# Optimization experiments

Measured on AMD Instinct MI355X. Metric: run time of the kernel, lower is better.

Reference implementation:

```python
import jax, jax.numpy as jnp
import numpy as np

SEG_LENS = (2048, 4096, 8192)
DIL_RATES = (1, 2, 4)
NUM_HEADS = 12
HEAD_DIM = 64
LN_EPS = 1e-5


def _dilated_attention(q, k, v):
    # q,k,v: [b, n, h, d]; heads partitioned across (segment, dilation) groups
    b, n, h, d = q.shape
    G = len(SEG_LENS)
    hg = h // G
    scale = d ** -0.5
    out = jnp.zeros_like(q)
    for i, (s, r) in enumerate(zip(SEG_LENS, DIL_RATES)):
        hmin = i * hg
        m = n // s                      # number of segments
        idx = jnp.arange(i % r, s, r)   # dilated positions within a segment, len = s // r
        def seg(t):
            # [b, n, hg, d] -> [b, m, s//r, hg, d]
            return t[:, :, hmin:hmin + hg, :].reshape(b, m, s, hg, d)[:, :, idx]
        qs, ks, vs = seg(q), seg(k), seg(v)
        scores = jnp.einsum('bmshd,bmthd->bmhst', qs, ks) * scale  # [b,m,hg,s/r,s/r]
        attn = jax.nn.softmax(scores, axis=-1)
        o = jnp.einsum('bmhst,bmthd->bmshd', attn, vs)              # [b,m,s/r,hg,d]
        pos = (jnp.arange(m)[:, None] * s + idx[None, :]).reshape(-1)
        out = out.at[:, pos, hmin:hmin + hg, :].set(o.reshape(b, -1, hg, d))
    return out


def setup_inputs() -> dict:
    key = jax.random.key(0)
    ks = jax.random.split(key, 4)
    E = NUM_HEADS * HEAD_DIM
    b, n = 1, 8192
    x = jax.random.normal(ks[0], (b, n, E), dtype=jnp.float32)
    w_qkv = jax.random.normal(ks[1], (3 * E, E), dtype=jnp.float32) * (E ** -0.5)
    b_qkv = jnp.zeros((3 * E,), dtype=jnp.float32)
    w_out = jax.random.normal(ks[2], (E, E), dtype=jnp.float32) * (E ** -0.5)
    b_out = jnp.zeros((E,), dtype=jnp.float32)
    ln_gamma = jnp.ones((E,), dtype=jnp.float32)
    ln_beta = jnp.zeros((E,), dtype=jnp.float32)
    return {'x': x, 'w_qkv': w_qkv, 'b_qkv': b_qkv, 'w_out': w_out,
            'b_out': b_out, 'ln_gamma': ln_gamma, 'ln_beta': ln_beta}


def reference(x, w_qkv, b_qkv, w_out, b_out, ln_gamma, ln_beta):
    b, n, E = x.shape
    qkv = x @ w_qkv.T + b_qkv
    q, k, v = jnp.split(qkv, 3, axis=-1)
    shp = (b, n, NUM_HEADS, HEAD_DIM)
    o = _dilated_attention(q.reshape(shp), k.reshape(shp), v.reshape(shp)).reshape(b, n, E)
    # MAGNETO: LayerNorm on attention output before out projection
    mu = jnp.mean(o, axis=-1, keepdims=True)
    var = jnp.mean(jnp.square(o - mu), axis=-1, keepdims=True)
    on = (o - mu) / jnp.sqrt(var + LN_EPS) * ln_gamma + ln_beta
    return on @ w_out.T + b_out
```

## Files before the change

kernel.cpp:

```cpp
#include <hip/hip_runtime.h>
#include <hip/hip_bf16.h>
#include <cstdint>
#include <cstddef>


typedef __attribute__((ext_vector_type(8))) short short8;
typedef __attribute__((ext_vector_type(4))) short short4_;
typedef __attribute__((ext_vector_type(4))) float float4_;

#if __has_builtin(__builtin_amdgcn_exp2f)
#define EXP2(x) __builtin_amdgcn_exp2f(x)
#else
#define EXP2(x) exp2f(x)
#endif

__device__ __forceinline__ float bf2f(short s) {
    unsigned int u = ((unsigned int)(unsigned short)s) << 16;
    float f;
    __builtin_memcpy(&f, &u, 4);
    return f;
}
__device__ __forceinline__ short f2bf(float f) {
    unsigned int u;
    __builtin_memcpy(&u, &f, 4);
    u += 0x7fffu + ((u >> 16) & 1u);
    return (short)(u >> 16);
}
__device__ __forceinline__ short f2bf_trunc(float f) {
    unsigned int u;
    __builtin_memcpy(&u, &f, 4);
    return (short)(u >> 16);
}
__device__ __forceinline__ short8 f8_to_bf8(const float* __restrict__ p) {
    float4_ a = *(const float4_*)(p);
    float4_ b = *(const float4_*)(p + 4);
    short8 r;
    r[0] = f2bf(a[0]); r[1] = f2bf(a[1]); r[2] = f2bf(a[2]); r[3] = f2bf(a[3]);
    r[4] = f2bf(b[0]); r[5] = f2bf(b[1]); r[6] = f2bf(b[2]); r[7] = f2bf(b[3]);
    return r;
}
__device__ __forceinline__ void gll16(const short* g, short* l) {
    __builtin_amdgcn_global_load_lds(
        (const __attribute__((address_space(1))) unsigned int*)g,
        (__attribute__((address_space(3))) unsigned int*)l, 16, 0, 0);
}

#define LDT 72

__global__ __launch_bounds__(256) void cvt3(
    const float* __restrict__ a, int na, const float* __restrict__ b, int nb,
    const float* __restrict__ c, int nc,
    short* __restrict__ oa, short* __restrict__ ob, short* __restrict__ oc)
{
    int i = (blockIdx.x * 256 + threadIdx.x) * 8;
    if (i < na) {
        *(short8*)&oa[i] = f8_to_bf8(a + i);
    } else if (i < na + nb) {
        int j = i - na;
        *(short8*)&ob[j] = f8_to_bf8(b + j);
    } else {
        int j = i - na - nb;
        if (j < nc) *(short8*)&oc[j] = f8_to_bf8(c + j);
    }
}

template<int EPI>
__global__ __launch_bounds__(256) void gemm128(
    const short* __restrict__ A, int lda,
    const short* __restrict__ B,
    const float* __restrict__ bias,
    void* __restrict__ Cv,
    int N, int K)
{
    __shared__ short As[128 * 64];
    __shared__ short Bs[128 * 64];
    const int tid  = threadIdx.x;
    const int wave = tid >> 6, lane = tid & 63;
    const int quad = lane >> 4, l16 = lane & 15;
    const int wr = wave >> 1, wc = wave & 1;
    const int m0 = blockIdx.y * 128, n0 = blockIdx.x * 128;
    const int lrow   = lane >> 3;
    const int lchunk = (lane & 7) ^ lrow;

    const short* Abase = A + (size_t)(m0 + wave * 32 + lrow) * lda + lchunk * 8;
    const short* Bbase = B + (size_t)(n0 + wave * 32 + lrow) * (size_t)K + lchunk * 8;
    short* AsW = &As[(wave * 32) * 64];
    short* BsW = &Bs[(wave * 32) * 64];

    float4_ acc[4][4] = {};

    for (int k0 = 0; k0 < K; k0 += 64) {
        __syncthreads();
        #pragma unroll
        for (int i = 0; i < 4; i++) {
            gll16(Abase + (size_t)(i * 8) * lda + k0, AsW + (i * 8) * 64);
            gll16(Bbase + (size_t)(i * 8) * K   + k0, BsW + (i * 8) * 64);
        }
        __syncthreads();
        #pragma unroll
        for (int ks = 0; ks < 2; ks++) {
            short8 af[4], bf[4];
            const int ca = ((ks * 4 + quad) ^ (l16 & 7)) * 8;
            #pragma unroll
            for (int t = 0; t < 4; t++) {
                af[t] = *(const short8*)&As[(wr * 64 + t * 16 + l16) * 64 + ca];
                bf[t] = *(const short8*)&Bs[(wc * 64 + t * 16 + l16) * 64 + ca];
            }
            #pragma unroll
            for (int mt = 0; mt < 4; mt++)
                #pragma unroll
                for (int nt = 0; nt < 4; nt++)
                    acc[mt][nt] = __builtin_amdgcn_mfma_f32_16x16x32_bf16(
                        af[mt], bf[nt], acc[mt][nt], 0, 0, 0);
        }
    }

    #pragma unroll
    for (int nt = 0; nt < 4; nt++) {
        const int col = n0 + wc * 64 + nt * 16 + l16;
        const float bv = bias[col];
        if constexpr (EPI == 0) {
            short* C = (short*)Cv;
            const int g = col >> 8;
            #pragma unroll
            for (int mt = 0; mt < 4; mt++) {
                #pragma unroll
                for (int r = 0; r < 4; r++) {
                    int row = m0 + wr * 64 + mt * 16 + quad * 4 + r;
                    bool cov = (col >= 768) || (g == 0) ||
                               (g == 1 && (row & 1) == 1) ||
                               (g == 2 && (row & 3) == 2);
                    C[(size_t)row * N + col] = cov ? f2bf(acc[mt][nt][r] + bv) : (short)0;
                }
            }
        } else {
            float* C = (float*)Cv;
            #pragma unroll
            for (int mt = 0; mt < 4; mt++)
                #pragma unroll
                for (int r = 0; r < 4; r++) {
                    int row = m0 + wr * 64 + mt * 16 + quad * 4 + r;
                    C[(size_t)row * N + col] = acc[mt][nt][r] + bv;
                }
        }
    }
}

__global__ __launch_bounds__(256, 3) void dilated_attn(
    short* __restrict__ qkv, float* __restrict__ lbuf)
{
    __shared__ short Ks[2 * 64 * 64];
    __shared__ short Vt[2 * 64 * LDT];
    __shared__ short Ps[4 * 32 * LDT];

    const int bx = blockIdx.x;
    const int qt = bx & 15;
    const int sh = bx >> 4;

    int g, seg, s, rate, off0;
    if (sh < 16)      { g = 0; seg = sh >> 2;        s = 2048; rate = 1; off0 = 0; }
    else if (sh < 24) { g = 1; seg = (sh - 16) >> 2; s = 4096; rate = 2; off0 = 1; }
    else              { g = 2; seg = 0;              s = 8192; rate = 4; off0 = 2; }
    const int head = g * 4 + (sh & 3);

    const int tid  = threadIdx.x;
    const int wave = tid >> 6, lane = tid & 63, quad = lane >> 4, l16 = lane & 15;
    const int srow = tid >> 2, scol = (tid & 3) * 16;

    short8 aq[2][2];
    #pragma unroll
    for (int rg = 0; rg < 2; rg++) {
        int t = qt * 128 + wave * 32 + rg * 16 + l16;
        size_t pos = (size_t)seg * s + off0 + (size_t)t * rate;
        const short* qsrc = qkv + pos * 2304 + head * 64 + quad * 8;
        #pragma unroll
        for (int ks = 0; ks < 2; ks++) {
            short8 q = *(const short8*)(qsrc + ks * 32);
            #pragma unroll
            for (int e = 0; e < 8; e++) q[e] = f2bf(bf2f(q[e]) * 0.1803368801111244f);
            aq[rg][ks] = q;
        }
    }

    const int krow0  = wave * 8 + (lane >> 3);
    const int kchunk = (lane & 7) ^ (lane >> 3);
    const size_t kstep = (size_t)64 * rate * 2304;
    const short* kg0 = qkv + ((size_t)seg * s + off0 + (size_t)krow0 * rate) * 2304
                           + 768 + head * 64 + kchunk * 8;
    const short* kg1 = kg0 + (size_t)32 * rate * 2304;
    const short* vgp = qkv + ((size_t)seg * s + off0 + (size_t)srow * rate) * 2304
                           + 1536 + head * 64 + scol;
    const int kofsA = (wave * 8) * 64;
    const int kofsB = kofsA + 32 * 64;
    const int vswz  = scol;

    gll16(kg0, &Ks[kofsA]);
    gll16(kg1, &Ks[kofsB]);
    kg0 += kstep; kg1 += kstep;
    short8 va0 = *(const short8*)(vgp);
    short8 va1 = *(const short8*)(vgp + 8);
    vgp += kstep;
    #pragma unroll
    for (int e = 0; e < 8; e++) Vt[(scol + e) * LDT + (srow ^ vswz)] = va0[e];
    #pragma unroll
    for (int e = 0; e < 8; e++) Vt[(scol + 8 + e) * LDT + (srow ^ vswz)] = va1[e];
    va0 = *(const short8*)(vgp);
    va1 = *(const short8*)(vgp + 8);
    vgp += kstep;

    float lrow[2][4] = {};
    float4_ oacc[2][4] = {};
    short* pw = &Ps[wave * 32 * LDT];
    const int cswap = (lane >> 5) & 1;
    const int pswz  = (l16 & 8) << 1;

    for (int j = 0; j < 32; j++) {
        __syncthreads();
        if (j < 31) {
            const int nb = (j + 1) & 1;
            gll16(kg0, &Ks[nb * 4096 + kofsA]);
            gll16(kg1, &Ks[nb * 4096 + kofsB]);
            kg0 += kstep; kg1 += kstep;
            short* vt = &Vt[nb * 64 * LDT];
            #pragma unroll
            for (int e = 0; e < 8; e++) vt[(scol + e) * LDT + (srow ^ vswz)] = va0[e];
            #pragma unroll
            for (int e = 0; e < 8; e++) vt[(scol + 8 + e) * LDT + (srow ^ vswz)] = va1[e];
            if (j < 30) {
                va0 = *(const short8*)(vgp);
                va1 = *(const short8*)(vgp + 8);
                vgp += kstep;
            }
        }
        const short* kb = &Ks[(j & 1) * 4096];
        const short* vb = &Vt[(j & 1) * 64 * LDT];

        float4_ sacc[2][4] = {};
        #pragma unroll
        for (int ks = 0; ks < 2; ks++) {
            #pragma unroll
            for (int kt = 0; kt < 4; kt++) {
                short8 bk = *(const short8*)&kb[(kt * 16 + l16) * 64
                                                + (((quad + 4 * ks) ^ (l16 & 7)) * 8)];
                #pragma unroll
                for (int rg = 0; rg < 2; rg++)
                    sacc[rg][kt] = __builtin_amdgcn_mfma_f32_16x16x32_bf16(
                        aq[rg][ks], bk, sacc[rg][kt], 0, 0, 0);
            }
        }

        #pragma unroll
        for (int rg = 0; rg < 2; rg++) {
            #pragma unroll
            for (int r = 0; r < 4; r++) {
                float p0 = EXP2(sacc[rg][0][r]), p1 = EXP2(sacc[rg][1][r]);
                float p2 = EXP2(sacc[rg][2][r]), p3 = EXP2(sacc[rg][3][r]);
                short* prow = &pw[(rg * 16 + quad * 4 + r) * LDT + l16];
                prow[(0 ^ cswap) * 16] = f2bf_trunc(p0);
                prow[(1 ^ cswap) * 16] = f2bf_trunc(p1);
                prow[(2 ^ cswap) * 16] = f2bf_trunc(p2);
                prow[(3 ^ cswap) * 16] = f2bf_trunc(p3);
                lrow[rg][r] += (p0 + p1) + (p2 + p3);
            }
        }

        #pragma unroll
        for (int ks = 0; ks < 2; ks++) {
            short8 ap[2];
            #pragma unroll
            for (int rg = 0; rg < 2; rg++)
                ap[rg] = *(const short8*)&pw[(rg * 16 + l16) * LDT
                                             + ((ks * 32 + quad * 8) ^ pswz)];
            #pragma unroll
            for (int nt = 0; nt < 4; nt++) {
                short8 bv = *(const short8*)&vb[(nt * 16 + l16) * LDT
                                                + ((ks * 32 + quad * 8) ^ (nt * 16))];
                #pragma unroll
                for (int rg = 0; rg < 2; rg++)
                    oacc[rg][nt] = __builtin_amdgcn_mfma_f32_16x16x32_bf16(
                        ap[rg], bv, oacc[rg][nt], 0, 0, 0);
            }
        }
    }

    #pragma unroll
    for (int rg = 0; rg < 2; rg++) {
        #pragma unroll
        for (int r = 0; r < 4; r++) {
            float v = lrow[rg][r];
            #pragma unroll
            for (int off = 1; off < 16; off <<= 1) v += __shfl_xor(v, off, 64);
            int qrow = wave * 32 + rg * 16 + quad * 4 + r;
            int t = qt * 128 + qrow;
            size_t pos = (size_t)seg * s + off0 + (size_t)t * rate;
            short* od = qkv + pos * 2304 + head * 64;
            #pragma unroll
            for (int nt = 0; nt < 4; nt++)
                od[nt * 16 + l16] = f2bf(oacc[rg][nt][r]);
            if (l16 == 0) lbuf[pos * 12 + head] = 1.0f / v;
        }
    }
}

__global__ __launch_bounds__(256) void ln_inplace(
    short* __restrict__ qkv, const float* __restrict__ lbuf,
    const float* __restrict__ gamma, const float* __restrict__ beta)
{
    const int row  = blockIdx.x * 4 + (threadIdx.x >> 6);
    const int lane = threadIdx.x & 63;
    short* src = qkv + (size_t)row * 2304;

    const float li1 = lbuf[row * 12 + (lane >> 3)];
    const float li2 = lbuf[row * 12 + 8 + (lane >> 4)];

    short8  a = *(const short8*)&src[lane * 8];
    short4_ b = *(const short4_*)&src[512 + lane * 4];
    float v[12];
    #pragma unroll
    for (int e = 0; e < 8; e++) v[e] = bf2f(a[e]) * li1;
    #pragma unroll
    for (int e = 0; e < 4; e++) v[8 + e] = bf2f(b[e]) * li2;

    float sum = 0.f, sq = 0.f;
    #pragma unroll
    for (int e = 0; e < 12; e++) { sum += v[e]; sq += v[e] * v[e]; }
    #pragma unroll
    for (int off = 1; off < 64; off <<= 1) {
        sum += __shfl_xor(sum, off, 64);
        sq  += __shfl_xor(sq,  off, 64);
    }
    float mean = sum * (1.0f / 768.0f);
    float var  = sq * (1.0f / 768.0f) - mean * mean;
    float rstd = rsqrtf(var + 1e-5f);

    short8 o8; short4_ o4;
    #pragma unroll
    for (int e = 0; e < 8; e++)
        o8[e] = f2bf((v[e] - mean) * rstd * gamma[lane * 8 + e] + beta[lane * 8 + e]);
    #pragma unroll
    for (int e = 0; e < 4; e++)
        o4[e] = f2bf((v[8 + e] - mean) * rstd * gamma[512 + lane * 4 + e] + beta[512 + lane * 4 + e]);

    *(short8*)&src[lane * 8] = o8;
    *(short4_*)&src[512 + lane * 4] = o4;
}

extern "C" void kernel_launch(void* const* d_in, const int* in_sizes, int n_in,
                              void* d_out, int out_size, void* d_ws, size_t ws_size,
                              hipStream_t stream) {
    const float* x     = (const float*)d_in[0];
    const float* w_qkv = (const float*)d_in[1];
    const float* b_qkv = (const float*)d_in[2];
    const float* w_out = (const float*)d_in[3];
    const float* b_out = (const float*)d_in[4];
    const float* gamma = (const float*)d_in[5];
    const float* beta  = (const float*)d_in[6];
    float* out = (float*)d_out;

    const int NX = 8192 * 768, NW1 = 2304 * 768, NW2 = 768 * 768;
    char* ws = (char*)d_ws;
    short* qkv   = (short*)(ws);
    short* xb    = (short*)(ws + (size_t)8192 * 2304 * 2);
    short* wqkvb = xb + NX;
    short* woutb = wqkvb + NW1;
    float* lbuf  = (float*)(woutb + NW2);

    cvt3<<<dim3((NX + NW1 + NW2) / (256 * 8)), 256, 0, stream>>>(
        x, NX, w_qkv, NW1, w_out, NW2, xb, wqkvb, woutb);

    gemm128<0><<<dim3(2304 / 128, 8192 / 128), 256, 0, stream>>>(
        xb, 768, wqkvb, b_qkv, qkv, 2304, 768);

    dilated_attn<<<dim3(28 * 16), 256, 0, stream>>>(qkv, lbuf);

    ln_inplace<<<dim3(8192 / 4), 256, 0, stream>>>(qkv, lbuf, gamma, beta);

    gemm128<1><<<dim3(768 / 128, 8192 / 128), 256, 0, stream>>>(
        qkv, 2304, woutb, b_out, out, 768, 768);
}
```

Measured before the change: 217.3 us.

## Split attention block across 8 waves with 16 query rows each

The attention kernel now launches 512 threads per block. Each of 8 waves handles 16 query rows instead of 4 waves handling 32 rows, so K/V tile loading is spread over more threads and each thread has fewer accumulator registers. MFMA sections are wrapped in s_setprio so waves in their matrix phase are favoured by the scheduler. Block indices are also permuted so neighbouring block IDs map to different segments and heads. The trade-off is less B-fragment reuse per wave, since each K/V LDS read now feeds one MFMA instead of two, plus more barrier participants per block.

Result: slower. 224.4 us (+3.3%).

```diff
diff --git a/kernel.cpp b/kernel.cpp
--- a/kernel.cpp
+++ b/kernel.cpp
@@ -146,16 +146,17 @@
     }
 }
 
-__global__ __launch_bounds__(256, 3) void dilated_attn(
+__global__ __launch_bounds__(512, 4) void dilated_attn(
     short* __restrict__ qkv, float* __restrict__ lbuf)
 {
     __shared__ short Ks[2 * 64 * 64];
     __shared__ short Vt[2 * 64 * LDT];
-    __shared__ short Ps[4 * 32 * LDT];
+    __shared__ short Ps[8 * 16 * LDT];
 
     const int bx = blockIdx.x;
-    const int qt = bx & 15;
-    const int sh = bx >> 4;
+    const int L  = (bx & 7) * 56 + (bx >> 3);
+    const int qt = L & 15;
+    const int sh = L >> 4;
 
     int g, seg, s, rate, off0;
     if (sh < 16)      { g = 0; seg = sh >> 2;        s = 2048; rate = 1; off0 = 0; }
@@ -165,12 +166,12 @@
 
     const int tid  = threadIdx.x;
     const int wave = tid >> 6, lane = tid & 63, quad = lane >> 4, l16 = lane & 15;
-    const int srow = tid >> 2, scol = (tid & 3) * 16;
-
-    short8 aq[2][2];
-    #pragma unroll
-    for (int rg = 0; rg < 2; rg++) {
-        int t = qt * 128 + wave * 32 + rg * 16 + l16;
+    const int srow = tid >> 3, scol = (tid & 7) * 8;
+    const int vswz = scol & 48;
+
+    short8 aq[2];
+    {
+        int t = qt * 128 + wave * 16 + l16;
         size_t pos = (size_t)seg * s + off0 + (size_t)t * rate;
         const short* qsrc = qkv + pos * 2304 + head * 64 + quad * 8;
         #pragma unroll
@@ -178,39 +179,31 @@
             short8 q = *(const short8*)(qsrc + ks * 32);
             #pragma unroll
             for (int e = 0; e < 8; e++) q[e] = f2bf(bf2f(q[e]) * 0.1803368801111244f);
-            aq[rg][ks] = q;
+            aq[ks] = q;
         }
     }
 
     const int krow0  = wave * 8 + (lane >> 3);
     const int kchunk = (lane & 7) ^ (lane >> 3);
     const size_t kstep = (size_t)64 * rate * 2304;
-    const short* kg0 = qkv + ((size_t)seg * s + off0 + (size_t)krow0 * rate) * 2304
-                           + 768 + head * 64 + kchunk * 8;
-    const short* kg1 = kg0 + (size_t)32 * rate * 2304;
+    const short* kg = qkv + ((size_t)seg * s + off0 + (size_t)krow0 * rate) * 2304
+                          + 768 + head * 64 + kchunk * 8;
     const short* vgp = qkv + ((size_t)seg * s + off0 + (size_t)srow * rate) * 2304
                            + 1536 + head * 64 + scol;
-    const int kofsA = (wave * 8) * 64;
-    const int kofsB = kofsA + 32 * 64;
-    const int vswz  = scol;
-
-    gll16(kg0, &Ks[kofsA]);
-    gll16(kg1, &Ks[kofsB]);
-    kg0 += kstep; kg1 += kstep;
-    short8 va0 = *(const short8*)(vgp);
-    short8 va1 = *(const short8*)(vgp + 8);
+    const int kofs = (wave * 8) * 64;
+
+    gll16(kg, &Ks[kofs]);
+    kg += kstep;
+    short8 va = *(const short8*)(vgp);
     vgp += kstep;
     #pragma unroll
-    for (int e = 0; e < 8; e++) Vt[(scol + e) * LDT + (srow ^ vswz)] = va0[e];
-    #pragma unroll
-    for (int e = 0; e < 8; e++) Vt[(scol + 8 + e) * LDT + (srow ^ vswz)] = va1[e];
-    va0 = *(const short8*)(vgp);
-    va1 = *(const short8*)(vgp + 8);
+    for (int e = 0; e < 8; e++) Vt[(scol + e) * LDT + (srow ^ vswz)] = va[e];
+    va = *(const short8*)(vgp);
     vgp += kstep;
 
-    float lrow[2][4] = {};
-    float4_ oacc[2][4] = {};
-    short* pw = &Ps[wave * 32 * LDT];
+    float lrow[4] = {};
+    float4_ oacc[4] = {};
+    short* pw = &Ps[wave * 16 * LDT];
     const int cswap = (lane >> 5) & 1;
     const int pswz  = (l16 & 8) << 1;
 
@@ -218,87 +211,73 @@
         __syncthreads();
         if (j < 31) {
             const int nb = (j + 1) & 1;
-            gll16(kg0, &Ks[nb * 4096 + kofsA]);
-            gll16(kg1, &Ks[nb * 4096 + kofsB]);
-            kg0 += kstep; kg1 += kstep;
+            gll16(kg, &Ks[nb * 4096 + kofs]);
+            kg += kstep;
             short* vt = &Vt[nb * 64 * LDT];
             #pragma unroll
-            for (int e = 0; e < 8; e++) vt[(scol + e) * LDT + (srow ^ vswz)] = va0[e];
-            #pragma unroll
-            for (int e = 0; e < 8; e++) vt[(scol + 8 + e) * LDT + (srow ^ vswz)] = va1[e];
+            for (int e = 0; e < 8; e++) vt[(scol + e) * LDT + (srow ^ vswz)] = va[e];
             if (j < 30) {
-                va0 = *(const short8*)(vgp);
-                va1 = *(const short8*)(vgp + 8);
+                va = *(const short8*)(vgp);
                 vgp += kstep;
             }
         }
         const short* kb = &Ks[(j & 1) * 4096];
         const short* vb = &Vt[(j & 1) * 64 * LDT];
 
-        float4_ sacc[2][4] = {};
+        float4_ sacc[4] = {};
+        __builtin_amdgcn_s_setprio(1);
         #pragma unroll
         for (int ks = 0; ks < 2; ks++) {
             #pragma unroll
             for (int kt = 0; kt < 4; kt++) {
                 short8 bk = *(const short8*)&kb[(kt * 16 + l16) * 64
                                                 + (((quad + 4 * ks) ^ (l16 & 7)) * 8)];
-                #pragma unroll
-                for (int rg = 0; rg < 2; rg++)
-                    sacc[rg][kt] = __builtin_amdgcn_mfma_f32_16x16x32_bf16(
-                        aq[rg][ks], bk, sacc[rg][kt], 0, 0, 0);
-            }
-        }
-
-        #pragma unroll
-        for (int rg = 0; rg < 2; rg++) {
-            #pragma unroll
-            for (int r = 0; r < 4; r++) {
-                float p0 = EXP2(sacc[rg][0][r]), p1 = EXP2(sacc[rg][1][r]);
-                float p2 = EXP2(sacc[rg][2][r]), p3 = EXP2(sacc[rg][3][r]);
-                short* prow = &pw[(rg * 16 + quad * 4 + r) * LDT + l16];
-                prow[(0 ^ cswap) * 16] = f2bf_trunc(p0);
-                prow[(1 ^ cswap) * 16] = f2bf_trunc(p1);
-                prow[(2 ^ cswap) * 16] = f2bf_trunc(p2);
-                prow[(3 ^ cswap) * 16] = f2bf_trunc(p3);
-                lrow[rg][r] += (p0 + p1) + (p2 + p3);
-            }
-        }
-
+                sacc[kt] = __builtin_amdgcn_mfma_f32_16x16x32_bf16(
+                    aq[ks], bk, sacc[kt], 0, 0, 0);
+            }
+        }
+        __builtin_amdgcn_s_setprio(0);
+
+        #pragma unroll
+        for (int r = 0; r < 4; r++) {
+            float p0 = EXP2(sacc[0][r]), p1 = EXP2(sacc[1][r]);
+            float p2 = EXP2(sacc[2][r]), p3 = EXP2(sacc[3][r]);
+            short* prow = &pw[(quad * 4 + r) * LDT + l16];
+            prow[(0 ^ cswap) * 16] = f2bf_trunc(p0);
+            prow[(1 ^ cswap) * 16] = f2bf_trunc(p1);
+            prow[(2 ^ cswap) * 16] = f2bf_trunc(p2);
+            prow[(3 ^ cswap) * 16] = f2bf_trunc(p3);
+            lrow[r] += (p0 + p1) + (p2 + p3);
+        }
+
+        __builtin_amdgcn_s_setprio(1);
         #pragma unroll
         for (int ks = 0; ks < 2; ks++) {
-            short8 ap[2];
-            #pragma unroll
-            for (int rg = 0; rg < 2; rg++)
-                ap[rg] = *(const short8*)&pw[(rg * 16 + l16) * LDT
-                                             + ((ks * 32 + quad * 8) ^ pswz)];
+            short8 ap = *(const short8*)&pw[l16 * LDT + ((ks * 32 + quad * 8) ^ pswz)];
             #pragma unroll
             for (int nt = 0; nt < 4; nt++) {
                 short8 bv = *(const short8*)&vb[(nt * 16 + l16) * LDT
                                                 + ((ks * 32 + quad * 8) ^ (nt * 16))];
-                #pragma unroll
-                for (int rg = 0; rg < 2; rg++)
-                    oacc[rg][nt] = __builtin_amdgcn_mfma_f32_16x16x32_bf16(
-                        ap[rg], bv, oacc[rg][nt], 0, 0, 0);
-            }
-        }
-    }
-
-    #pragma unroll
-    for (int rg = 0; rg < 2; rg++) {
-        #pragma unroll
-        for (int r = 0; r < 4; r++) {
-            float v = lrow[rg][r];
-            #pragma unroll
-            for (int off = 1; off < 16; off <<= 1) v += __shfl_xor(v, off, 64);
-            int qrow = wave * 32 + rg * 16 + quad * 4 + r;
-            int t = qt * 128 + qrow;
-            size_t pos = (size_t)seg * s + off0 + (size_t)t * rate;
-            short* od = qkv + pos * 2304 + head * 64;
-            #pragma unroll
-            for (int nt = 0; nt < 4; nt++)
-                od[nt * 16 + l16] = f2bf(oacc[rg][nt][r]);
-            if (l16 == 0) lbuf[pos * 12 + head] = 1.0f / v;
-        }
+                oacc[nt] = __builtin_amdgcn_mfma_f32_16x16x32_bf16(
+                    ap, bv, oacc[nt], 0, 0, 0);
+            }
+        }
+        __builtin_amdgcn_s_setprio(0);
+    }
+
+    #pragma unroll
+    for (int r = 0; r < 4; r++) {
+        float v = lrow[r];
+        #pragma unroll
+        for (int off = 1; off < 16; off <<= 1) v += __shfl_xor(v, off, 64);
+        int qrow = wave * 16 + quad * 4 + r;
+        int t = qt * 128 + qrow;
+        size_t pos = (size_t)seg * s + off0 + (size_t)t * rate;
+        short* od = qkv + pos * 2304 + head * 64;
+        #pragma unroll
+        for (int nt = 0; nt < 4; nt++)
+            od[nt * 16 + l16] = f2bf(oacc[nt][r]);
+        if (l16 == 0) lbuf[pos * 12 + head] = 1.0f / v;
     }
 }
 
@@ -371,7 +350,7 @@
     gemm128<0><<<dim3(2304 / 128, 8192 / 128), 256, 0, stream>>>(
         xb, 768, wqkvb, b_qkv, qkv, 2304, 768);
 
-    dilated_attn<<<dim3(28 * 16), 256, 0, stream>>>(qkv, lbuf);
+    dilated_attn<<<dim3(28 * 16), 512, 0, stream>>>(qkv, lbuf);
 
     ln_inplace<<<dim3(8192 / 4), 256, 0, stream>>>(qkv, lbuf, gamma, beta);
 
```

## Split attention key range across two blocks and merge partials in LayerNorm

Applied to the files above, without the earlier changes.

Each (segment, head, query-tile) attention block now covers only half of the keys, which doubles the grid to 896 blocks. The first half writes its unnormalised output in place into the q columns of qkv. The second half writes to a separate buffer that reuses the freed xb region. Both halves write raw row sums to separate lbuf halves, and the LayerNorm kernel adds the two partials and normalises. Combining this way is valid because the softmax uses exp2 without max subtraction. The change also remaps block indices across XCDs and raises wave priority around the MFMA sections. The aim is better CU occupancy than the under-filled 448-block grid, at the cost of redundant Q loads and a possible race: the second-half block reads the same Q rows that the first-half block overwrites when it finishes.

Result: no change. 220.1 us (+1.3%).

```diff
diff --git a/kernel.cpp b/kernel.cpp
--- a/kernel.cpp
+++ b/kernel.cpp
@@ -147,15 +147,17 @@
 }
 
 __global__ __launch_bounds__(256, 3) void dilated_attn(
-    short* __restrict__ qkv, float* __restrict__ lbuf)
+    short* __restrict__ qkv, short* __restrict__ obuf2, float* __restrict__ lbuf)
 {
     __shared__ short Ks[2 * 64 * 64];
     __shared__ short Vt[2 * 64 * LDT];
     __shared__ short Ps[4 * 32 * LDT];
 
     const int bx = blockIdx.x;
-    const int qt = bx & 15;
-    const int sh = bx >> 4;
+    const int L  = (bx & 7) * 112 + (bx >> 3);
+    const int qt   = L & 15;
+    const int half = (L >> 4) & 1;
+    const int sh   = L >> 5;
 
     int g, seg, s, rate, off0;
     if (sh < 16)      { g = 0; seg = sh >> 2;        s = 2048; rate = 1; off0 = 0; }
@@ -185,10 +187,11 @@
     const int krow0  = wave * 8 + (lane >> 3);
     const int kchunk = (lane & 7) ^ (lane >> 3);
     const size_t kstep = (size_t)64 * rate * 2304;
-    const short* kg0 = qkv + ((size_t)seg * s + off0 + (size_t)krow0 * rate) * 2304
+    const size_t kq0 = (size_t)seg * s + off0 + (size_t)(half * 1024) * rate;
+    const short* kg0 = qkv + (kq0 + (size_t)krow0 * rate) * 2304
                            + 768 + head * 64 + kchunk * 8;
     const short* kg1 = kg0 + (size_t)32 * rate * 2304;
-    const short* vgp = qkv + ((size_t)seg * s + off0 + (size_t)srow * rate) * 2304
+    const short* vgp = qkv + (kq0 + (size_t)srow * rate) * 2304
                            + 1536 + head * 64 + scol;
     const int kofsA = (wave * 8) * 64;
     const int kofsB = kofsA + 32 * 64;
@@ -214,9 +217,9 @@
     const int cswap = (lane >> 5) & 1;
     const int pswz  = (l16 & 8) << 1;
 
-    for (int j = 0; j < 32; j++) {
+    for (int j = 0; j < 16; j++) {
         __syncthreads();
-        if (j < 31) {
+        if (j < 15) {
             const int nb = (j + 1) & 1;
             gll16(kg0, &Ks[nb * 4096 + kofsA]);
             gll16(kg1, &Ks[nb * 4096 + kofsB]);
@@ -226,7 +229,7 @@
             for (int e = 0; e < 8; e++) vt[(scol + e) * LDT + (srow ^ vswz)] = va0[e];
             #pragma unroll
             for (int e = 0; e < 8; e++) vt[(scol + 8 + e) * LDT + (srow ^ vswz)] = va1[e];
-            if (j < 30) {
+            if (j < 14) {
                 va0 = *(const short8*)(vgp);
                 va1 = *(const short8*)(vgp + 8);
                 vgp += kstep;
@@ -236,6 +239,7 @@
         const short* vb = &Vt[(j & 1) * 64 * LDT];
 
         float4_ sacc[2][4] = {};
+        __builtin_amdgcn_s_setprio(1);
         #pragma unroll
         for (int ks = 0; ks < 2; ks++) {
             #pragma unroll
@@ -248,6 +252,7 @@
                         aq[rg][ks], bk, sacc[rg][kt], 0, 0, 0);
             }
         }
+        __builtin_amdgcn_s_setprio(0);
 
         #pragma unroll
         for (int rg = 0; rg < 2; rg++) {
@@ -264,6 +269,7 @@
             }
         }
 
+        __builtin_amdgcn_s_setprio(1);
         #pragma unroll
         for (int ks = 0; ks < 2; ks++) {
             short8 ap[2];
@@ -281,8 +287,12 @@
                         ap[rg], bv, oacc[rg][nt], 0, 0, 0);
             }
         }
-    }
-
+        __builtin_amdgcn_s_setprio(0);
+    }
+
+    short* obase = half ? obuf2 : qkv;
+    const int ostride = half ? 768 : 2304;
+    float* lb = lbuf + (size_t)half * 8192 * 12;
     #pragma unroll
     for (int rg = 0; rg < 2; rg++) {
         #pragma unroll
@@ -293,33 +303,45 @@
             int qrow = wave * 32 + rg * 16 + quad * 4 + r;
             int t = qt * 128 + qrow;
             size_t pos = (size_t)seg * s + off0 + (size_t)t * rate;
-            short* od = qkv + pos * 2304 + head * 64;
+            short* od = obase + pos * ostride + head * 64;
             #pragma unroll
             for (int nt = 0; nt < 4; nt++)
                 od[nt * 16 + l16] = f2bf(oacc[rg][nt][r]);
-            if (l16 == 0) lbuf[pos * 12 + head] = 1.0f / v;
+            if (l16 == 0) lb[pos * 12 + head] = v;
         }
     }
 }
 
 __global__ __launch_bounds__(256) void ln_inplace(
-    short* __restrict__ qkv, const float* __restrict__ lbuf,
+    short* __restrict__ qkv, const short* __restrict__ obuf2,
+    const float* __restrict__ lbuf,
     const float* __restrict__ gamma, const float* __restrict__ beta)
 {
     const int row  = blockIdx.x * 4 + (threadIdx.x >> 6);
     const int lane = threadIdx.x & 63;
     short* src = qkv + (size_t)row * 2304;
-
-    const float li1 = lbuf[row * 12 + (lane >> 3)];
-    const float li2 = lbuf[row * 12 + 8 + (lane >> 4)];
-
-    short8  a = *(const short8*)&src[lane * 8];
-    short4_ b = *(const short4_*)&src[512 + lane * 4];
+    const short* src2 = obuf2 + (size_t)row * 768;
+
+    const int h1 = lane >> 3;
+    const int h2 = 8 + (lane >> 4);
+    const bool cov1 = (h1 < 4) || ((row & 1) == 1);
+    const bool cov2 = ((row & 3) == 2);
+    const float li1 = cov1
+        ? 1.0f / (lbuf[row * 12 + h1] + lbuf[8192 * 12 + row * 12 + h1]) : 0.0f;
+    const float li2 = cov2
+        ? 1.0f / (lbuf[row * 12 + h2] + lbuf[8192 * 12 + row * 12 + h2]) : 0.0f;
+
+    short8  a  = *(const short8*)&src[lane * 8];
+    short4_ b  = *(const short4_*)&src[512 + lane * 4];
+    short8  a2 = *(const short8*)&src2[lane * 8];
+    short4_ b2 = *(const short4_*)&src2[512 + lane * 4];
     float v[12];
     #pragma unroll
-    for (int e = 0; e < 8; e++) v[e] = bf2f(a[e]) * li1;
-    #pragma unroll
-    for (int e = 0; e < 4; e++) v[8 + e] = bf2f(b[e]) * li2;
+    for (int e = 0; e < 8; e++)
+        v[e] = cov1 ? (bf2f(a[e]) + bf2f(a2[e])) * li1 : 0.0f;
+    #pragma unroll
+    for (int e = 0; e < 4; e++)
+        v[8 + e] = cov2 ? (bf2f(b[e]) + bf2f(b2[e])) * li2 : 0.0f;
 
     float sum = 0.f, sq = 0.f;
     #pragma unroll
@@ -364,6 +386,7 @@
     short* wqkvb = xb + NX;
     short* woutb = wqkvb + NW1;
     float* lbuf  = (float*)(woutb + NW2);
+    short* obuf2 = xb;
 
     cvt3<<<dim3((NX + NW1 + NW2) / (256 * 8)), 256, 0, stream>>>(
         x, NX, w_qkv, NW1, w_out, NW2, xb, wqkvb, woutb);
@@ -371,9 +394,9 @@
     gemm128<0><<<dim3(2304 / 128, 8192 / 128), 256, 0, stream>>>(
         xb, 768, wqkvb, b_qkv, qkv, 2304, 768);
 
-    dilated_attn<<<dim3(28 * 16), 256, 0, stream>>>(qkv, lbuf);
-
-    ln_inplace<<<dim3(8192 / 4), 256, 0, stream>>>(qkv, lbuf, gamma, beta);
+    dilated_attn<<<dim3(28 * 2 * 16), 256, 0, stream>>>(qkv, obuf2, lbuf);
+
+    ln_inplace<<<dim3(8192 / 4), 256, 0, stream>>>(qkv, obuf2, lbuf, gamma, beta);
 
     gemm128<1><<<dim3(768 / 128, 8192 / 128), 256, 0, stream>>>(
         qkv, 2304, woutb, b_out, out, 768, 768);
```

## Use 32x32 MFMA with register-resident P via permlane swap in dilated attention

Applied to the files above, without the earlier changes.

Switches the attention inner loop from 16x16x32 to 32x32x16 bf16 MFMAs, computing S^T so the exponentiated probabilities can be packed with v_cvt_pk_bf16_f32 and rearranged with v_permlane32_swap instead of going through a shared-memory P buffer. This removes the LDS round trip and the Ps allocation, and adds s_setprio around the MFMA blocks plus a remapped block order. The row-sum reciprocal moves into the LayerNorm kernel, which also masks head slots that are not covered by the dilation pattern. It relies on gfx950-specific instructions and a more intricate lane mapping.

After: 213.4 us. Within noise of the previous version (-1.8%).

```diff
diff --git a/kernel.cpp b/kernel.cpp
--- a/kernel.cpp
+++ b/kernel.cpp
@@ -7,6 +7,8 @@
 typedef __attribute__((ext_vector_type(8))) short short8;
 typedef __attribute__((ext_vector_type(4))) short short4_;
 typedef __attribute__((ext_vector_type(4))) float float4_;
+typedef __attribute__((ext_vector_type(16))) float floatx16;
+typedef __attribute__((ext_vector_type(4))) int int4_;
 
 #if __has_builtin(__builtin_amdgcn_exp2f)
 #define EXP2(x) __builtin_amdgcn_exp2f(x)
@@ -24,11 +26,6 @@
     unsigned int u;
     __builtin_memcpy(&u, &f, 4);
     u += 0x7fffu + ((u >> 16) & 1u);
-    return (short)(u >> 16);
-}
-__device__ __forceinline__ short f2bf_trunc(float f) {
-    unsigned int u;
-    __builtin_memcpy(&u, &f, 4);
     return (short)(u >> 16);
 }
 __device__ __forceinline__ short8 f8_to_bf8(const float* __restrict__ p) {
@@ -43,6 +40,11 @@
     __builtin_amdgcn_global_load_lds(
         (const __attribute__((address_space(1))) unsigned int*)g,
         (__attribute__((address_space(3))) unsigned int*)l, 16, 0, 0);
+}
+__device__ __forceinline__ int cvtpk(float lo, float hi) {
+    int r;
+    asm("v_cvt_pk_bf16_f32 %0, %1, %2" : "=v"(r) : "v"(lo), "v"(hi));
+    return r;
 }
 
 #define LDT 72
@@ -151,11 +153,11 @@
 {
     __shared__ short Ks[2 * 64 * 64];
     __shared__ short Vt[2 * 64 * LDT];
-    __shared__ short Ps[4 * 32 * LDT];
 
     const int bx = blockIdx.x;
-    const int qt = bx & 15;
-    const int sh = bx >> 4;
+    const int L  = (bx & 7) * 56 + (bx >> 3);
+    const int qt = L & 15;
+    const int sh = L >> 4;
 
     int g, seg, s, rate, off0;
     if (sh < 16)      { g = 0; seg = sh >> 2;        s = 2048; rate = 1; off0 = 0; }
@@ -164,21 +166,22 @@
     const int head = g * 4 + (sh & 3);
 
     const int tid  = threadIdx.x;
-    const int wave = tid >> 6, lane = tid & 63, quad = lane >> 4, l16 = lane & 15;
+    const int wave = tid >> 6, lane = tid & 63;
+    const int h = lane >> 5, l32 = lane & 31;
     const int srow = tid >> 2, scol = (tid & 3) * 16;
 
-    short8 aq[2][2];
-    #pragma unroll
-    for (int rg = 0; rg < 2; rg++) {
-        int t = qt * 128 + wave * 32 + rg * 16 + l16;
-        size_t pos = (size_t)seg * s + off0 + (size_t)t * rate;
-        const short* qsrc = qkv + pos * 2304 + head * 64 + quad * 8;
-        #pragma unroll
-        for (int ks = 0; ks < 2; ks++) {
-            short8 q = *(const short8*)(qsrc + ks * 32);
+    const size_t bpos = (size_t)seg * s + off0
+                      + (size_t)(qt * 128 + wave * 32) * rate;
+    short8 aq[4];
+    {
+        const short* qsrc = qkv + (bpos + (size_t)l32 * rate) * 2304
+                                + head * 64 + h * 8;
+        #pragma unroll
+        for (int kt = 0; kt < 4; kt++) {
+            short8 q = *(const short8*)(qsrc + kt * 16);
             #pragma unroll
             for (int e = 0; e < 8; e++) q[e] = f2bf(bf2f(q[e]) * 0.1803368801111244f);
-            aq[rg][ks] = q;
+            aq[kt] = q;
         }
     }
 
@@ -208,11 +211,8 @@
     va1 = *(const short8*)(vgp + 8);
     vgp += kstep;
 
-    float lrow[2][4] = {};
-    float4_ oacc[2][4] = {};
-    short* pw = &Ps[wave * 32 * LDT];
-    const int cswap = (lane >> 5) & 1;
-    const int pswz  = (l16 & 8) << 1;
+    float lsum = 0.f;
+    floatx16 oacc[2] = {};
 
     for (int j = 0; j < 32; j++) {
         __syncthreads();
@@ -235,70 +235,71 @@
         const short* kb = &Ks[(j & 1) * 4096];
         const short* vb = &Vt[(j & 1) * 64 * LDT];
 
-        float4_ sacc[2][4] = {};
-        #pragma unroll
-        for (int ks = 0; ks < 2; ks++) {
-            #pragma unroll
-            for (int kt = 0; kt < 4; kt++) {
-                short8 bk = *(const short8*)&kb[(kt * 16 + l16) * 64
-                                                + (((quad + 4 * ks) ^ (l16 & 7)) * 8)];
-                #pragma unroll
-                for (int rg = 0; rg < 2; rg++)
-                    sacc[rg][kt] = __builtin_amdgcn_mfma_f32_16x16x32_bf16(
-                        aq[rg][ks], bk, sacc[rg][kt], 0, 0, 0);
-            }
-        }
-
-        #pragma unroll
-        for (int rg = 0; rg < 2; rg++) {
+        floatx16 sacc[2] = {};
+        __builtin_amdgcn_s_setprio(1);
+        #pragma unroll
+        for (int kt = 0; kt < 4; kt++) {
+            #pragma unroll
+            for (int t = 0; t < 2; t++) {
+                short8 ak = *(const short8*)&kb[(t * 32 + l32) * 64
+                                                + (((kt * 2 + h) ^ (l32 & 7)) * 8)];
+                sacc[t] = __builtin_amdgcn_mfma_f32_32x32x16_bf16(
+                    ak, aq[kt], sacc[t], 0, 0, 0);
+            }
+        }
+        __builtin_amdgcn_s_setprio(0);
+
+        #pragma unroll
+        for (int e = 0; e < 16; e++) {
+            float pa_ = EXP2(sacc[0][e]);
+            float pb_ = EXP2(sacc[1][e]);
+            sacc[0][e] = pa_; sacc[1][e] = pb_;
+            lsum += pa_ + pb_;
+        }
+
+        short8 pa[4];
+        #pragma unroll
+        for (int kt = 0; kt < 4; kt++) {
+            const int t = kt >> 1, b = (kt & 1) * 8;
+            int A1 = cvtpk(sacc[t][b + 0], sacc[t][b + 1]);
+            int A2 = cvtpk(sacc[t][b + 2], sacc[t][b + 3]);
+            int B1 = cvtpk(sacc[t][b + 4], sacc[t][b + 5]);
+            int B2 = cvtpk(sacc[t][b + 6], sacc[t][b + 7]);
+            asm volatile("v_permlane32_swap_b32 %0, %1" : "+v"(A1), "+v"(B1));
+            asm volatile("v_permlane32_swap_b32 %0, %1" : "+v"(A2), "+v"(B2));
+            int4_ w; w[0] = A1; w[1] = A2; w[2] = B1; w[3] = B2;
+            __builtin_memcpy(&pa[kt], &w, 16);
+        }
+
+        __builtin_amdgcn_s_setprio(1);
+        #pragma unroll
+        for (int kt = 0; kt < 4; kt++) {
+            #pragma unroll
+            for (int dt = 0; dt < 2; dt++) {
+                const int d = dt * 32 + l32;
+                short8 bv = *(const short8*)&vb[d * LDT
+                                                + ((kt ^ ((d >> 4) & 3)) * 16 + h * 8)];
+                oacc[dt] = __builtin_amdgcn_mfma_f32_32x32x16_bf16(
+                    pa[kt], bv, oacc[dt], 0, 0, 0);
+            }
+        }
+        __builtin_amdgcn_s_setprio(0);
+    }
+
+    {
+        float lt = lsum + __shfl_xor(lsum, 32, 64);
+        #pragma unroll
+        for (int m = 0; m < 4; m++) {
             #pragma unroll
             for (int r = 0; r < 4; r++) {
-                float p0 = EXP2(sacc[rg][0][r]), p1 = EXP2(sacc[rg][1][r]);
-                float p2 = EXP2(sacc[rg][2][r]), p3 = EXP2(sacc[rg][3][r]);
-                short* prow = &pw[(rg * 16 + quad * 4 + r) * LDT + l16];
-                prow[(0 ^ cswap) * 16] = f2bf_trunc(p0);
-                prow[(1 ^ cswap) * 16] = f2bf_trunc(p1);
-                prow[(2 ^ cswap) * 16] = f2bf_trunc(p2);
-                prow[(3 ^ cswap) * 16] = f2bf_trunc(p3);
-                lrow[rg][r] += (p0 + p1) + (p2 + p3);
-            }
-        }
-
-        #pragma unroll
-        for (int ks = 0; ks < 2; ks++) {
-            short8 ap[2];
-            #pragma unroll
-            for (int rg = 0; rg < 2; rg++)
-                ap[rg] = *(const short8*)&pw[(rg * 16 + l16) * LDT
-                                             + ((ks * 32 + quad * 8) ^ pswz)];
-            #pragma unroll
-            for (int nt = 0; nt < 4; nt++) {
-                short8 bv = *(const short8*)&vb[(nt * 16 + l16) * LDT
-                                                + ((ks * 32 + quad * 8) ^ (nt * 16))];
-                #pragma unroll
-                for (int rg = 0; rg < 2; rg++)
-                    oacc[rg][nt] = __builtin_amdgcn_mfma_f32_16x16x32_bf16(
-                        ap[rg], bv, oacc[rg][nt], 0, 0, 0);
-            }
-        }
-    }
-
-    #pragma unroll
-    for (int rg = 0; rg < 2; rg++) {
-        #pragma unroll
-        for (int r = 0; r < 4; r++) {
-            float v = lrow[rg][r];
-            #pragma unroll
-            for (int off = 1; off < 16; off <<= 1) v += __shfl_xor(v, off, 64);
-            int qrow = wave * 32 + rg * 16 + quad * 4 + r;
-            int t = qt * 128 + qrow;
-            size_t pos = (size_t)seg * s + off0 + (size_t)t * rate;
-            short* od = qkv + pos * 2304 + head * 64;
-            #pragma unroll
-            for (int nt = 0; nt < 4; nt++)
-                od[nt * 16 + l16] = f2bf(oacc[rg][nt][r]);
-            if (l16 == 0) lbuf[pos * 12 + head] = 1.0f / v;
-        }
+                const int ql = 4 * h + r + 8 * m;
+                short* od = qkv + (bpos + (size_t)ql * rate) * 2304 + head * 64;
+                od[l32]      = f2bf(oacc[0][m * 4 + r]);
+                od[32 + l32] = f2bf(oacc[1][m * 4 + r]);
+            }
+        }
+        if (lane < 32)
+            lbuf[(bpos + (size_t)l32 * rate) * 12 + head] = lt;
     }
 }
 
@@ -310,8 +311,12 @@
     const int lane = threadIdx.x & 63;
     short* src = qkv + (size_t)row * 2304;
 
-    const float li1 = lbuf[row * 12 + (lane >> 3)];
-    const float li2 = lbuf[row * 12 + 8 + (lane >> 4)];
+    const int h1 = lane >> 3;
+    const int h2 = 8 + (lane >> 4);
+    const bool cov1 = (h1 < 4) || ((row & 1) == 1);
+    const bool cov2 = ((row & 3) == 2);
+    const float li1 = cov1 ? 1.0f / lbuf[row * 12 + h1] : 0.0f;
+    const float li2 = cov2 ? 1.0f / lbuf[row * 12 + h2] : 0.0f;
 
     short8  a = *(const short8*)&src[lane * 8];
     short4_ b = *(const short4_*)&src[512 + lane * 4];
```
